# Performance work log

Measured on AMD Instinct MI355X. Metric: run time of the kernel, lower is better.

## Reference

```python
import jax, jax.numpy as jnp
import numpy as np

IN_DIM = 128
NUM_KERNELS = 512
OUT_DIM = 256
EPS_NORM = 1e-09


def setup_inputs() -> dict:
    key = jax.random.key(0)
    k1, k2, k3, k4 = jax.random.split(key, 4)
    inp = jax.random.normal(k1, (16, 512, IN_DIM), dtype=jnp.float32)
    # centers ~ U[-1, 1] as in reset(upper_bound_kernels=1.0)
    centers = jax.random.uniform(k2, (NUM_KERNELS, IN_DIM), dtype=jnp.float32, minval=-1.0, maxval=1.0)
    # log shapes ~ N(0, 0.1)
    log_shapes = 0.1 * jax.random.normal(k3, (NUM_KERNELS,), dtype=jnp.float32)
    # xavier-uniform weights, gain=1: bound = sqrt(6/(fan_in+fan_out))
    bound = float(np.sqrt(6.0 / (NUM_KERNELS + OUT_DIM)))
    weights = jax.random.uniform(k4, (OUT_DIM, NUM_KERNELS), dtype=jnp.float32, minval=-bound, maxval=bound)
    return {"input": inp, "kernels_centers": centers, "log_shapes": log_shapes, "weights": weights}


def reference(input, kernels_centers, log_shapes, weights):
    lead = input.shape[:-1]
    x = input.reshape(-1, input.shape[-1])            # (N, D)
    diff = x[:, None, :] - kernels_centers[None, :, :]  # (N, K, D)
    r = jnp.linalg.norm(diff, axis=-1)                 # (N, K)
    eps_r = jnp.exp(log_shapes)[None, :] * r           # (N, K)
    rbfs = jnp.exp(-eps_r ** 2)                        # gaussian RBF
    rbfs = rbfs / (jnp.sum(rbfs, axis=-1, keepdims=True) + EPS_NORM)
    out = rbfs @ weights.T                             # (N, OUT)
    return out.reshape(lead + (weights.shape[0],))
```

## Files before the change

### kernel.cpp

```cpp
#include <hip/hip_runtime.h>

typedef float  f32x4 __attribute__((ext_vector_type(4)));
typedef short  s16x8 __attribute__((ext_vector_type(8)));
typedef ushort u16x8 __attribute__((ext_vector_type(8)));

constexpr int D  = 128;
constexpr int K  = 512;
constexpr int O  = 256;
constexpr int NT = 256;
constexpr float NL2E = -1.44269504088896340736f;

__device__ __forceinline__ ushort f2bf(float f) {
    uint u = __builtin_bit_cast(uint, f);
    return (ushort)((u + 0x7FFFu + ((u >> 16) & 1u)) >> 16);
}
__device__ __forceinline__ float bf2f(ushort h) {
    return __builtin_bit_cast(float, ((uint)h) << 16);
}

__global__ __launch_bounds__(NT)
void rbf_prep(const float* __restrict__ x, const float* __restrict__ cen,
              const float* __restrict__ ls, const float* __restrict__ w,
              ushort* __restrict__ Xh, ushort* __restrict__ Xl,
              ushort* __restrict__ Ch, ushort* __restrict__ Cl,
              ushort* __restrict__ Wf, float* __restrict__ xs2,
              float2* __restrict__ ecs, int nxb, int ncb)
{
    __shared__ float red[4][16];
    const int b = blockIdx.x, t = threadIdx.x, lane = t & 63, wq = t >> 6;

    if (b < nxb + ncb) {
        const bool isX  = b < nxb;
        const int panel = isX ? b : (b - nxb);
        const float* src = isX ? x : cen;
        ushort* dh = isX ? Xh : Ch;
        ushort* dl = isX ? Xl : Cl;
        const int row = panel * 16 + (lane & 15);
        const int col = wq * 32 + (lane >> 4) * 8;
        const float* p = src + (size_t)row * D + col;
        float4 v0 = *(const float4*)p, v1 = *(const float4*)(p + 4);
        float f[8] = {v0.x, v0.y, v0.z, v0.w, v1.x, v1.y, v1.z, v1.w};
        u16x8 h, l;
        float s = 0.f;
#pragma unroll
        for (int j = 0; j < 8; ++j) {
            s = fmaf(f[j], f[j], s);
            ushort hb = f2bf(f[j]);
            h[j] = hb;
            l[j] = f2bf(f[j] - bf2f(hb));
        }
        const size_t c = ((size_t)panel * 4 + wq) * 64 + lane;
        *(u16x8*)&dh[c * 8] = h;
        *(u16x8*)&dl[c * 8] = l;
        s += __shfl_xor(s, 16);
        s += __shfl_xor(s, 32);
        if (lane < 16) red[wq][lane] = s;
        __syncthreads();
        if (t < 16) {
            float sum = red[0][t] + red[1][t] + red[2][t] + red[3][t];
            if (isX) {
                xs2[panel * 16 + t] = sum;
            } else {
                int k = panel * 16 + t;
                float e = __expf(2.0f * ls[k]);
                ecs[k] = make_float2(NL2E * e, NL2E * e * sum);
            }
        }
    } else {
        const int c0 = (b - nxb - ncb) * NT + t;
        const int ln = c0 & 63, ot = (c0 >> 6) & 15, ks = c0 >> 10;
        const int o  = ot * 16 + (ln & 15);
        const int kb = ks * 32 + (ln >> 4) * 8;
        const float* p = w + (size_t)o * K + kb;
        float4 v0 = *(const float4*)p, v1 = *(const float4*)(p + 4);
        u16x8 h;
        h[0] = f2bf(v0.x); h[1] = f2bf(v0.y); h[2] = f2bf(v0.z); h[3] = f2bf(v0.w);
        h[4] = f2bf(v1.x); h[5] = f2bf(v1.y); h[6] = f2bf(v1.z); h[7] = f2bf(v1.w);
        *(u16x8*)&Wf[(size_t)c0 * 8] = h;
    }
}

constexpr int PP = 40;

__global__ __launch_bounds__(512, 1)
void rbf_main2p(const ushort* __restrict__ Xh, const ushort* __restrict__ Xl,
                const ushort* __restrict__ Ch, const ushort* __restrict__ Cl,
                const ushort* __restrict__ Wf, const float* __restrict__ xs2,
                const float2* __restrict__ ecs, float* __restrict__ out, int N)
{
    __shared__ ushort PsA[8][16][PP];
    __shared__ ushort PsB[8][16][PP];
    __shared__ float  Acc[2][32][O + 4];
    __shared__ float  Ls[8][32];

    const int t = threadIdx.x, lane = t & 63, wv = t >> 6;
    const int l15 = lane & 15, l4 = lane >> 4;
    const int pan = blockIdx.x;

    s16x8 xhA[4], xlA[4], xhB[4], xlB[4];
    {
        const size_t baseA = ((size_t)(pan * 2) * 4) * 64 + lane;
        const size_t baseB = ((size_t)(pan * 2 + 1) * 4) * 64 + lane;
#pragma unroll
        for (int q = 0; q < 4; ++q) {
            xhA[q] = *(const s16x8*)&Xh[(baseA + q * 64) * 8];
            xlA[q] = *(const s16x8*)&Xl[(baseA + q * 64) * 8];
            xhB[q] = *(const s16x8*)&Xh[(baseB + q * 64) * 8];
            xlB[q] = *(const s16x8*)&Xl[(baseB + q * 64) * 8];
        }
    }
    const float xs2A = xs2[pan * 32 + l15];
    const float xs2B = xs2[pan * 32 + 16 + l15];

    f32x4 oaccA[16], oaccB[16];
#pragma unroll
    for (int i = 0; i < 16; ++i) {
        oaccA[i] = (f32x4){0.f, 0.f, 0.f, 0.f};
        oaccB[i] = (f32x4){0.f, 0.f, 0.f, 0.f};
    }
    float LpA = 0.f, LpB = 0.f;

    const int kw = wv * 64;

#pragma unroll
    for (int s = 0; s < 2; ++s) {
        const int kslab = (kw >> 5) + s;
        const ushort* wbase = &Wf[(((size_t)kslab * 16) * 64 + lane) * 8];

#pragma unroll
        for (int bt = 0; bt < 2; ++bt) {
            const size_t kt16 = (size_t)(kw >> 4) + s * 2 + bt;
            s16x8 ch[4], cl[4];
#pragma unroll
            for (int q = 0; q < 4; ++q) {
                const size_t cc = ((kt16 * 4 + q) * 64 + lane) * 8;
                ch[q] = *(const s16x8*)&Ch[cc];
                cl[q] = *(const s16x8*)&Cl[cc];
            }
            f32x4 gA = (f32x4){0.f,0.f,0.f,0.f};
            f32x4 gB = (f32x4){0.f,0.f,0.f,0.f};
#pragma unroll
            for (int q = 0; q < 4; ++q) {
                gA = __builtin_amdgcn_mfma_f32_16x16x32_bf16(ch[q], xhA[q], gA, 0, 0, 0);
                gB = __builtin_amdgcn_mfma_f32_16x16x32_bf16(ch[q], xhB[q], gB, 0, 0, 0);
            }
#pragma unroll
            for (int q = 0; q < 4; ++q) {
                gA = __builtin_amdgcn_mfma_f32_16x16x32_bf16(ch[q], xlA[q], gA, 0, 0, 0);
                gB = __builtin_amdgcn_mfma_f32_16x16x32_bf16(ch[q], xlB[q], gB, 0, 0, 0);
            }
#pragma unroll
            for (int q = 0; q < 4; ++q) {
                gA = __builtin_amdgcn_mfma_f32_16x16x32_bf16(cl[q], xhA[q], gA, 0, 0, 0);
                gB = __builtin_amdgcn_mfma_f32_16x16x32_bf16(cl[q], xhB[q], gB, 0, 0, 0);
            }

            const int kbase = kw + s * 32 + bt * 16 + l4 * 4;
            float4 e0 = *(const float4*)&ecs[kbase];
            float4 e1 = *(const float4*)&ecs[kbase + 2];
            {
                float p0 = exp2f(fmaf(e0.x, fmaf(-2.f, gA[0], xs2A), e0.y));
                float p1 = exp2f(fmaf(e0.z, fmaf(-2.f, gA[1], xs2A), e0.w));
                float p2 = exp2f(fmaf(e1.x, fmaf(-2.f, gA[2], xs2A), e1.y));
                float p3 = exp2f(fmaf(e1.z, fmaf(-2.f, gA[3], xs2A), e1.w));
                LpA += (p0 + p1) + (p2 + p3);
                uint u0 = (uint)f2bf(p0) | ((uint)f2bf(p1) << 16);
                uint u1 = (uint)f2bf(p2) | ((uint)f2bf(p3) << 16);
                *(uint2*)&PsA[wv][l15][bt * 16 + l4 * 4] = make_uint2(u0, u1);
            }
            {
                float p0 = exp2f(fmaf(e0.x, fmaf(-2.f, gB[0], xs2B), e0.y));
                float p1 = exp2f(fmaf(e0.z, fmaf(-2.f, gB[1], xs2B), e0.w));
                float p2 = exp2f(fmaf(e1.x, fmaf(-2.f, gB[2], xs2B), e1.y));
                float p3 = exp2f(fmaf(e1.z, fmaf(-2.f, gB[3], xs2B), e1.w));
                LpB += (p0 + p1) + (p2 + p3);
                uint u0 = (uint)f2bf(p0) | ((uint)f2bf(p1) << 16);
                uint u1 = (uint)f2bf(p2) | ((uint)f2bf(p3) << 16);
                *(uint2*)&PsB[wv][l15][bt * 16 + l4 * 4] = make_uint2(u0, u1);
            }
        }

        s16x8 paA = *(const s16x8*)&PsA[wv][l15][l4 * 8];
        s16x8 paB = *(const s16x8*)&PsB[wv][l15][l4 * 8];
#pragma unroll
        for (int ot = 0; ot < 16; ++ot) {
            s16x8 bfr = *(const s16x8*)&wbase[(size_t)ot * 64 * 8];
            oaccA[ot] = __builtin_amdgcn_mfma_f32_16x16x32_bf16(paA, bfr, oaccA[ot], 0, 0, 0);
            oaccB[ot] = __builtin_amdgcn_mfma_f32_16x16x32_bf16(paB, bfr, oaccB[ot], 0, 0, 0);
        }
    }

    {
        float vA = LpA, vB = LpB;
        vA += __shfl_xor(vA, 16);  vA += __shfl_xor(vA, 32);
        vB += __shfl_xor(vB, 16);  vB += __shfl_xor(vB, 32);
        if (lane < 16) {
            Ls[wv][lane]      = vA;
            Ls[wv][16 + lane] = vB;
        }
    }

    if (wv < 2) {
#pragma unroll
        for (int ot = 0; ot < 16; ++ot)
#pragma unroll
            for (int r = 0; r < 4; ++r) {
                Acc[wv][l4 * 4 + r][ot * 16 + l15]      = oaccA[ot][r];
                Acc[wv][16 + l4 * 4 + r][ot * 16 + l15] = oaccB[ot][r];
            }
    }
    __syncthreads();
    if (wv == 2 || wv == 3) {
#pragma unroll
        for (int ot = 0; ot < 16; ++ot)
#pragma unroll
            for (int r = 0; r < 4; ++r) {
                Acc[wv - 2][l4 * 4 + r][ot * 16 + l15]      += oaccA[ot][r];
                Acc[wv - 2][16 + l4 * 4 + r][ot * 16 + l15] += oaccB[ot][r];
            }
    }
    __syncthreads();
    if (wv == 4 || wv == 5) {
#pragma unroll
        for (int ot = 0; ot < 16; ++ot)
#pragma unroll
            for (int r = 0; r < 4; ++r) {
                Acc[wv - 4][l4 * 4 + r][ot * 16 + l15]      += oaccA[ot][r];
                Acc[wv - 4][16 + l4 * 4 + r][ot * 16 + l15] += oaccB[ot][r];
            }
    }
    __syncthreads();
    if (wv >= 6) {
#pragma unroll
        for (int ot = 0; ot < 16; ++ot)
#pragma unroll
            for (int r = 0; r < 4; ++r) {
                Acc[wv - 6][l4 * 4 + r][ot * 16 + l15]      += oaccA[ot][r];
                Acc[wv - 6][16 + l4 * 4 + r][ot * 16 + l15] += oaccB[ot][r];
            }
    }
    __syncthreads();

    {
        const int n  = t >> 4;
        const int c0 = (t & 15) * 16;
        float inv = 1.0f / (Ls[0][n] + Ls[1][n] + Ls[2][n] + Ls[3][n] +
                            Ls[4][n] + Ls[5][n] + Ls[6][n] + Ls[7][n] + 1e-9f);
        float* po = &out[(size_t)(pan * 32 + n) * O + c0];
#pragma unroll
        for (int j = 0; j < 4; ++j) {
            float4 a = *(const float4*)&Acc[0][n][c0 + j * 4];
            float4 b = *(const float4*)&Acc[1][n][c0 + j * 4];
            float4 o;
            o.x = (a.x + b.x) * inv;
            o.y = (a.y + b.y) * inv;
            o.z = (a.z + b.z) * inv;
            o.w = (a.w + b.w) * inv;
            *(float4*)(po + j * 4) = o;
        }
    }
}

__global__ __launch_bounds__(NT, 2)
void rbf_fb(const float* __restrict__ x, const float* __restrict__ cen,
            const float* __restrict__ ls, const float* __restrict__ w,
            float* __restrict__ out)
{
    __shared__ ushort Ps2[2][4][16][PP];
    __shared__ float  Acc2[2][16][O + 4];
    __shared__ float  Ls2[4][16];
    const int t = threadIdx.x, lane = t & 63, wv = t >> 6;
    const int l15 = lane & 15, l4 = lane >> 4;
    const int nb = blockIdx.x * 16;

    s16x8 xh[4], xl[4];
    float sx = 0.f;
    {
        const float* xr = x + (size_t)(nb + l15) * D;
#pragma unroll
        for (int q = 0; q < 4; ++q) {
            float4 v0 = *(const float4*)(xr + q * 32 + l4 * 8);
            float4 v1 = *(const float4*)(xr + q * 32 + l4 * 8 + 4);
            float f[8] = {v0.x, v0.y, v0.z, v0.w, v1.x, v1.y, v1.z, v1.w};
            s16x8 hh, lo;
#pragma unroll
            for (int j = 0; j < 8; ++j) {
                sx = fmaf(f[j], f[j], sx);
                ushort hb = f2bf(f[j]);
                hh[j] = (short)hb; lo[j] = (short)f2bf(f[j] - bf2f(hb));
            }
            xh[q] = hh; xl[q] = lo;
        }
    }
    sx += __shfl_xor(sx, 16); sx += __shfl_xor(sx, 32);
    float xs2v[4];
#pragma unroll
    for (int r = 0; r < 4; ++r) xs2v[r] = __shfl(sx, l4 * 4 + r);

    f32x4 oacc[16];
#pragma unroll
    for (int ot = 0; ot < 16; ++ot) oacc[ot] = (f32x4){0.f,0.f,0.f,0.f};
    float Lp[4] = {0.f,0.f,0.f,0.f};
    const int kq = wv * (K / 4);

#pragma unroll
    for (int s = 0; s < 4; ++s) {
        const int k0 = kq + s * 32;
#pragma unroll
        for (int bt = 0; bt < 2; ++bt) {
            const int kk = k0 + bt * 16 + l15;
            const float* cr = cen + (size_t)kk * D;
            s16x8 ch[4], cl[4];
            float sc = 0.f;
#pragma unroll
            for (int q = 0; q < 4; ++q) {
                float4 v0 = *(const float4*)(cr + q * 32 + l4 * 8);
                float4 v1 = *(const float4*)(cr + q * 32 + l4 * 8 + 4);
                float f[8] = {v0.x, v0.y, v0.z, v0.w, v1.x, v1.y, v1.z, v1.w};
                s16x8 hh, lo;
#pragma unroll
                for (int j = 0; j < 8; ++j) {
                    sc = fmaf(f[j], f[j], sc);
                    ushort hb = f2bf(f[j]);
                    hh[j] = (short)hb; lo[j] = (short)f2bf(f[j] - bf2f(hb));
                }
                ch[q] = hh; cl[q] = lo;
            }
            sc += __shfl_xor(sc, 16); sc += __shfl_xor(sc, 32);
            float es_ = __expf(2.0f * ls[kk]);
            f32x4 ghh={0,0,0,0}, ghl={0,0,0,0}, glh={0,0,0,0};
#pragma unroll
            for (int q = 0; q < 4; ++q) {
                ghh = __builtin_amdgcn_mfma_f32_16x16x32_bf16(xh[q], ch[q], ghh, 0,0,0);
                ghl = __builtin_amdgcn_mfma_f32_16x16x32_bf16(xh[q], cl[q], ghl, 0,0,0);
                glh = __builtin_amdgcn_mfma_f32_16x16x32_bf16(xl[q], ch[q], glh, 0,0,0);
            }
            f32x4 gg = ghh + ghl + glh;
#pragma unroll
            for (int r = 0; r < 4; ++r) {
                float r2 = xs2v[r] + sc - 2.0f * gg[r];
                float ph = __expf(-es_ * r2);
                Lp[r] += ph;
                Ps2[s & 1][wv][l4 * 4 + r][bt * 16 + l15] = f2bf(ph);
            }
        }
        s16x8 pa = *(const s16x8*)&Ps2[s & 1][wv][l15][l4 * 8];
#pragma unroll
        for (int ot = 0; ot < 16; ++ot) {
            const float* wr = w + (size_t)(ot * 16 + l15) * K + k0;
            float4 v0 = *(const float4*)(wr + l4 * 8);
            float4 v1 = *(const float4*)(wr + l4 * 8 + 4);
            s16x8 bb;
            bb[0]=(short)f2bf(v0.x); bb[1]=(short)f2bf(v0.y); bb[2]=(short)f2bf(v0.z); bb[3]=(short)f2bf(v0.w);
            bb[4]=(short)f2bf(v1.x); bb[5]=(short)f2bf(v1.y); bb[6]=(short)f2bf(v1.z); bb[7]=(short)f2bf(v1.w);
            oacc[ot] = __builtin_amdgcn_mfma_f32_16x16x32_bf16(pa, bb, oacc[ot], 0,0,0);
        }
    }
#pragma unroll
    for (int r = 0; r < 4; ++r) {
        float v = Lp[r];
        v += __shfl_xor(v, 1); v += __shfl_xor(v, 2);
        v += __shfl_xor(v, 4); v += __shfl_xor(v, 8);
        if (l15 == 0) Ls2[wv][l4 * 4 + r] = v;
    }
    if (wv < 2) {
#pragma unroll
        for (int ot = 0; ot < 16; ++ot)
#pragma unroll
            for (int r = 0; r < 4; ++r)
                Acc2[wv][l4 * 4 + r][ot * 16 + l15] = oacc[ot][r];
    }
    __syncthreads();
    if (wv >= 2) {
#pragma unroll
        for (int ot = 0; ot < 16; ++ot)
#pragma unroll
            for (int r = 0; r < 4; ++r)
                Acc2[wv - 2][l4 * 4 + r][ot * 16 + l15] += oacc[ot][r];
    }
    __syncthreads();
#pragma unroll
    for (int rr = 0; rr < 4; ++rr) {
        const int n = wv * 4 + rr;
        float inv = 1.0f / (Ls2[0][n] + Ls2[1][n] + Ls2[2][n] + Ls2[3][n] + 1e-9f);
        float4 a0 = *(const float4*)&Acc2[0][n][lane * 4];
        float4 a1 = *(const float4*)&Acc2[1][n][lane * 4];
        float4 o4;
        o4.x = (a0.x + a1.x) * inv; o4.y = (a0.y + a1.y) * inv;
        o4.z = (a0.z + a1.z) * inv; o4.w = (a0.w + a1.w) * inv;
        *(float4*)&out[(size_t)(nb + n) * O + lane * 4] = o4;
    }
}

extern "C" void kernel_launch(void* const* d_in, const int* in_sizes, int n_in,
                              void* d_out, int out_size, void* d_ws, size_t ws_size,
                              hipStream_t stream) {
    const float* x   = (const float*)d_in[0];
    const float* cen = (const float*)d_in[1];
    const float* ls  = (const float*)d_in[2];
    const float* w   = (const float*)d_in[3];
    float* out = (float*)d_out;
    const int N = in_sizes[0] / D;

    size_t oXh = 0;
    size_t oXl = oXh + (size_t)N * D * 2;
    size_t oCh = oXl + (size_t)N * D * 2;
    size_t oCl = oCh + (size_t)K * D * 2;
    size_t oWf = oCl + (size_t)K * D * 2;
    size_t oxs = oWf + (size_t)O * K * 2;
    size_t oec = oxs + (size_t)N * 4;
    size_t need = oec + (size_t)K * 8;

    if (ws_size < need || (N % 32) != 0) {
        dim3 grid(N / 16), block(NT);
        hipLaunchKernelGGL(rbf_fb, grid, block, 0, stream, x, cen, ls, w, out);
        return;
    }

    char* ws = (char*)d_ws;
    ushort* Xh = (ushort*)(ws + oXh);
    ushort* Xl = (ushort*)(ws + oXl);
    ushort* Ch = (ushort*)(ws + oCh);
    ushort* Cl = (ushort*)(ws + oCl);
    ushort* Wf = (ushort*)(ws + oWf);
    float*  xs2 = (float*)(ws + oxs);
    float2* ecs = (float2*)(ws + oec);

    const int nxb = N / 16;
    const int ncb = K / 16;
    const int nwb = (O * K / 8) / NT;
    dim3 pgrid(nxb + ncb + nwb), pblock(NT);
    hipLaunchKernelGGL(rbf_prep, pgrid, pblock, 0, stream,
                       x, cen, ls, w, Xh, Xl, Ch, Cl, Wf, xs2, ecs, nxb, ncb);

    dim3 grid(N / 32), block(512);
    hipLaunchKernelGGL(rbf_main2p, grid, block, 0, stream,
                       Xh, Xl, Ch, Cl, Wf, xs2, ecs, out, N);
}
```

Measured before the change: 27.76 us.

## Fuse prep and main kernels into one cooperative kernel with grid sync

Merges the preprocessing kernel (bf16 hi/lo splitting of inputs and centers, squared norms, weight conversion) and the main RBF/GEMM kernel into a single cooperative launch separated by a grid-wide barrier. This removes one kernel launch and the gap between the two kernels. The cooperative path is hardcoded to N=8192 (256 blocks, 608 prep jobs), and falls back to the two-kernel path if the cooperative launch fails. It depends on all 256 blocks of 512 threads being co-resident, and the grid sync adds its own cost.

```diff
diff --git a/kernel.cpp b/kernel.cpp
--- a/kernel.cpp
+++ b/kernel.cpp
@@ -1,4 +1,7 @@
 #include <hip/hip_runtime.h>
+#include <hip/hip_cooperative_groups.h>
+
+namespace cg = cooperative_groups;
 
 typedef float  f32x4 __attribute__((ext_vector_type(4)));
 typedef short  s16x8 __attribute__((ext_vector_type(8)));
@@ -16,6 +19,250 @@
 }
 __device__ __forceinline__ float bf2f(ushort h) {
     return __builtin_bit_cast(float, ((uint)h) << 16);
+}
+
+constexpr int PP = 40;
+
+__global__ __launch_bounds__(512, 1)
+void rbf_coop(const float* __restrict__ x, const float* __restrict__ cen,
+              const float* __restrict__ ls, const float* __restrict__ w,
+              ushort* __restrict__ Xh, ushort* __restrict__ Xl,
+              ushort* __restrict__ Ch, ushort* __restrict__ Cl,
+              ushort* __restrict__ Wf, float* __restrict__ xs2,
+              float2* __restrict__ ecs, float* __restrict__ out, int N)
+{
+    __shared__ ushort PsA[8][16][PP];
+    __shared__ ushort PsB[8][16][PP];
+    __shared__ float  Acc[2][32][O + 4];
+    __shared__ float  Ls[8][32];
+
+    const int tt = threadIdx.x;
+
+    {
+        const int hb   = blockIdx.x * 2 + (tt >> 8);
+        const int tloc = tt & 255;
+        const int wj = (tloc >> 6);
+        const int lj = tloc & 63;
+        const int rr = lj >> 4;
+        const int cb = lj & 15;
+        for (int job = hb; job < 608; job += 512) {
+            if (job < 544) {
+                const bool isX = job < 512;
+                const int panel = isX ? job : job - 512;
+                const float* src = isX ? x : cen;
+                ushort* dh = isX ? Xh : Ch;
+                ushort* dl = isX ? Xl : Cl;
+                const int row = panel * 16 + wj * 4 + rr;
+                const float* p = src + (size_t)row * D + cb * 8;
+                float4 v0 = *(const float4*)p, v1 = *(const float4*)(p + 4);
+                float f[8] = {v0.x, v0.y, v0.z, v0.w, v1.x, v1.y, v1.z, v1.w};
+                u16x8 h, l;
+                float s = 0.f;
+#pragma unroll
+                for (int j = 0; j < 8; ++j) {
+                    s = fmaf(f[j], f[j], s);
+                    ushort hb2 = f2bf(f[j]);
+                    h[j] = hb2;
+                    l[j] = f2bf(f[j] - bf2f(hb2));
+                }
+                const int q  = cb >> 2;
+                const int lp = (wj * 4 + rr) + (cb & 3) * 16;
+                const size_t c = ((size_t)panel * 4 + q) * 64 + lp;
+                *(u16x8*)&dh[c * 8] = h;
+                *(u16x8*)&dl[c * 8] = l;
+                s += __shfl_xor(s, 1); s += __shfl_xor(s, 2);
+                s += __shfl_xor(s, 4); s += __shfl_xor(s, 8);
+                if (cb == 0) {
+                    if (isX) {
+                        xs2[row] = s;
+                    } else {
+                        float e = __expf(2.0f * ls[row]);
+                        ecs[row] = make_float2(NL2E * e, NL2E * e * s);
+                    }
+                }
+            } else {
+                const int c0 = (job - 544) * 256 + tloc;
+                const int ln = c0 & 63, ot = (c0 >> 6) & 15, ks = c0 >> 10;
+                const int o  = ot * 16 + (ln & 15);
+                const int kb = ks * 32 + (ln >> 4) * 8;
+                const float* p = w + (size_t)o * K + kb;
+                float4 v0 = *(const float4*)p, v1 = *(const float4*)(p + 4);
+                u16x8 h;
+                h[0] = f2bf(v0.x); h[1] = f2bf(v0.y); h[2] = f2bf(v0.z); h[3] = f2bf(v0.w);
+                h[4] = f2bf(v1.x); h[5] = f2bf(v1.y); h[6] = f2bf(v1.z); h[7] = f2bf(v1.w);
+                *(u16x8*)&Wf[(size_t)c0 * 8] = h;
+            }
+        }
+    }
+
+    cg::this_grid().sync();
+
+    const int lane = tt & 63, wv = tt >> 6;
+    const int l15 = lane & 15, l4 = lane >> 4;
+    const int pan = blockIdx.x;
+
+    s16x8 xhA[4], xlA[4], xhB[4], xlB[4];
+    {
+        const size_t baseA = ((size_t)(pan * 2) * 4) * 64 + lane;
+        const size_t baseB = ((size_t)(pan * 2 + 1) * 4) * 64 + lane;
+#pragma unroll
+        for (int q = 0; q < 4; ++q) {
+            xhA[q] = *(const s16x8*)&Xh[(baseA + q * 64) * 8];
+            xlA[q] = *(const s16x8*)&Xl[(baseA + q * 64) * 8];
+            xhB[q] = *(const s16x8*)&Xh[(baseB + q * 64) * 8];
+            xlB[q] = *(const s16x8*)&Xl[(baseB + q * 64) * 8];
+        }
+    }
+    const float xs2A = xs2[pan * 32 + l15];
+    const float xs2B = xs2[pan * 32 + 16 + l15];
+
+    f32x4 oaccA[16], oaccB[16];
+#pragma unroll
+    for (int i = 0; i < 16; ++i) {
+        oaccA[i] = (f32x4){0.f, 0.f, 0.f, 0.f};
+        oaccB[i] = (f32x4){0.f, 0.f, 0.f, 0.f};
+    }
+    float LpA = 0.f, LpB = 0.f;
+
+    const int kw = wv * 64;
+
+#pragma unroll
+    for (int s = 0; s < 2; ++s) {
+        const int kslab = (kw >> 5) + s;
+        const ushort* wbase = &Wf[(((size_t)kslab * 16) * 64 + lane) * 8];
+
+#pragma unroll
+        for (int bt = 0; bt < 2; ++bt) {
+            const size_t kt16 = (size_t)(kw >> 4) + s * 2 + bt;
+            s16x8 ch[4], cl[4];
+#pragma unroll
+            for (int q = 0; q < 4; ++q) {
+                const size_t cc = ((kt16 * 4 + q) * 64 + lane) * 8;
+                ch[q] = *(const s16x8*)&Ch[cc];
+                cl[q] = *(const s16x8*)&Cl[cc];
+            }
+            f32x4 gA = (f32x4){0.f,0.f,0.f,0.f};
+            f32x4 gB = (f32x4){0.f,0.f,0.f,0.f};
+#pragma unroll
+            for (int q = 0; q < 4; ++q) {
+                gA = __builtin_amdgcn_mfma_f32_16x16x32_bf16(ch[q], xhA[q], gA, 0, 0, 0);
+                gB = __builtin_amdgcn_mfma_f32_16x16x32_bf16(ch[q], xhB[q], gB, 0, 0, 0);
+            }
+#pragma unroll
+            for (int q = 0; q < 4; ++q) {
+                gA = __builtin_amdgcn_mfma_f32_16x16x32_bf16(ch[q], xlA[q], gA, 0, 0, 0);
+                gB = __builtin_amdgcn_mfma_f32_16x16x32_bf16(ch[q], xlB[q], gB, 0, 0, 0);
+            }
+#pragma unroll
+            for (int q = 0; q < 4; ++q) {
+                gA = __builtin_amdgcn_mfma_f32_16x16x32_bf16(cl[q], xhA[q], gA, 0, 0, 0);
+                gB = __builtin_amdgcn_mfma_f32_16x16x32_bf16(cl[q], xhB[q], gB, 0, 0, 0);
+            }
+
+            const int kbase = kw + s * 32 + bt * 16 + l4 * 4;
+            float4 e0 = *(const float4*)&ecs[kbase];
+            float4 e1 = *(const float4*)&ecs[kbase + 2];
+            {
+                float p0 = exp2f(fmaf(e0.x, fmaf(-2.f, gA[0], xs2A), e0.y));
+                float p1 = exp2f(fmaf(e0.z, fmaf(-2.f, gA[1], xs2A), e0.w));
+                float p2 = exp2f(fmaf(e1.x, fmaf(-2.f, gA[2], xs2A), e1.y));
+                float p3 = exp2f(fmaf(e1.z, fmaf(-2.f, gA[3], xs2A), e1.w));
+                LpA += (p0 + p1) + (p2 + p3);
+                uint u0 = (uint)f2bf(p0) | ((uint)f2bf(p1) << 16);
+                uint u1 = (uint)f2bf(p2) | ((uint)f2bf(p3) << 16);
+                *(uint2*)&PsA[wv][l15][bt * 16 + l4 * 4] = make_uint2(u0, u1);
+            }
+            {
+                float p0 = exp2f(fmaf(e0.x, fmaf(-2.f, gB[0], xs2B), e0.y));
+                float p1 = exp2f(fmaf(e0.z, fmaf(-2.f, gB[1], xs2B), e0.w));
+                float p2 = exp2f(fmaf(e1.x, fmaf(-2.f, gB[2], xs2B), e1.y));
+                float p3 = exp2f(fmaf(e1.z, fmaf(-2.f, gB[3], xs2B), e1.w));
+                LpB += (p0 + p1) + (p2 + p3);
+                uint u0 = (uint)f2bf(p0) | ((uint)f2bf(p1) << 16);
+                uint u1 = (uint)f2bf(p2) | ((uint)f2bf(p3) << 16);
+                *(uint2*)&PsB[wv][l15][bt * 16 + l4 * 4] = make_uint2(u0, u1);
+            }
+        }
+
+        s16x8 paA = *(const s16x8*)&PsA[wv][l15][l4 * 8];
+        s16x8 paB = *(const s16x8*)&PsB[wv][l15][l4 * 8];
+#pragma unroll
+        for (int ot = 0; ot < 16; ++ot) {
+            s16x8 bfr = *(const s16x8*)&wbase[(size_t)ot * 64 * 8];
+            oaccA[ot] = __builtin_amdgcn_mfma_f32_16x16x32_bf16(paA, bfr, oaccA[ot], 0, 0, 0);
+            oaccB[ot] = __builtin_amdgcn_mfma_f32_16x16x32_bf16(paB, bfr, oaccB[ot], 0, 0, 0);
+        }
+    }
+
+    {
+        float vA = LpA, vB = LpB;
+        vA += __shfl_xor(vA, 16);  vA += __shfl_xor(vA, 32);
+        vB += __shfl_xor(vB, 16);  vB += __shfl_xor(vB, 32);
+        if (lane < 16) {
+            Ls[wv][lane]      = vA;
+            Ls[wv][16 + lane] = vB;
+        }
+    }
+
+    if (wv < 2) {
+#pragma unroll
+        for (int ot = 0; ot < 16; ++ot)
+#pragma unroll
+            for (int r = 0; r < 4; ++r) {
+                Acc[wv][l4 * 4 + r][ot * 16 + l15]      = oaccA[ot][r];
+                Acc[wv][16 + l4 * 4 + r][ot * 16 + l15] = oaccB[ot][r];
+            }
+    }
+    __syncthreads();
+    if (wv == 2 || wv == 3) {
+#pragma unroll
+        for (int ot = 0; ot < 16; ++ot)
+#pragma unroll
+            for (int r = 0; r < 4; ++r) {
+                Acc[wv - 2][l4 * 4 + r][ot * 16 + l15]      += oaccA[ot][r];
+                Acc[wv - 2][16 + l4 * 4 + r][ot * 16 + l15] += oaccB[ot][r];
+            }
+    }
+    __syncthreads();
+    if (wv == 4 || wv == 5) {
+#pragma unroll
+        for (int ot = 0; ot < 16; ++ot)
+#pragma unroll
+            for (int r = 0; r < 4; ++r) {
+                Acc[wv - 4][l4 * 4 + r][ot * 16 + l15]      += oaccA[ot][r];
+                Acc[wv - 4][16 + l4 * 4 + r][ot * 16 + l15] += oaccB[ot][r];
+            }
+    }
+    __syncthreads();
+    if (wv >= 6) {
+#pragma unroll
+        for (int ot = 0; ot < 16; ++ot)
+#pragma unroll
+            for (int r = 0; r < 4; ++r) {
+                Acc[wv - 6][l4 * 4 + r][ot * 16 + l15]      += oaccA[ot][r];
+                Acc[wv - 6][16 + l4 * 4 + r][ot * 16 + l15] += oaccB[ot][r];
+            }
+    }
+    __syncthreads();
+
+    {
+        const int n  = tt >> 4;
+        const int c0 = (tt & 15) * 16;
+        float inv = 1.0f / (Ls[0][n] + Ls[1][n] + Ls[2][n] + Ls[3][n] +
+                            Ls[4][n] + Ls[5][n] + Ls[6][n] + Ls[7][n] + 1e-9f);
+        float* po = &out[(size_t)(pan * 32 + n) * O + c0];
+#pragma unroll
+        for (int j = 0; j < 4; ++j) {
+            float4 a = *(const float4*)&Acc[0][n][c0 + j * 4];
+            float4 b = *(const float4*)&Acc[1][n][c0 + j * 4];
+            float4 o;
+            o.x = (a.x + b.x) * inv;
+            o.y = (a.y + b.y) * inv;
+            o.z = (a.z + b.z) * inv;
+            o.w = (a.w + b.w) * inv;
+            *(float4*)(po + j * 4) = o;
+        }
+    }
 }
 
 __global__ __launch_bounds__(NT)
@@ -80,8 +327,6 @@
     }
 }
 
-constexpr int PP = 40;
-
 __global__ __launch_bounds__(512, 1)
 void rbf_main2p(const ushort* __restrict__ Xh, const ushort* __restrict__ Xl,
                 const ushort* __restrict__ Ch, const ushort* __restrict__ Cl,
@@ -411,7 +656,7 @@
     size_t oec = oxs + (size_t)N * 4;
     size_t need = oec + (size_t)K * 8;
 
-    if (ws_size < need || (N % 32) != 0) {
+    if (ws_size < need || N != 8192) {
         dim3 grid(N / 16), block(NT);
         hipLaunchKernelGGL(rbf_fb, grid, block, 0, stream, x, cen, ls, w, out);
         return;
@@ -426,6 +671,19 @@
     float*  xs2 = (float*)(ws + oxs);
     float2* ecs = (float2*)(ws + oec);
 
+    {
+        int Nv = N;
+        void* params[] = { (void*)&x, (void*)&cen, (void*)&ls, (void*)&w,
+                           (void*)&Xh, (void*)&Xl, (void*)&Ch, (void*)&Cl,
+                           (void*)&Wf, (void*)&xs2, (void*)&ecs,
+                           (void*)&out, (void*)&Nv };
+        hipError_t err = hipLaunchCooperativeKernel(
+            reinterpret_cast<void*>(&rbf_coop), dim3(N / 32), dim3(512),
+            params, 0, stream);
+        if (err == hipSuccess) return;
+        (void)hipGetLastError();
+    }
+
     const int nxb = N / 16;
     const int ncb = K / 16;
     const int nwb = (O * K / 8) / NT;
```

Result: slower. 66.26 us (+138.7%).

## Fuse bf16 prep into main kernel, converting inputs on the fly

Applied to the files above, without the earlier changes.

Drops the separate prep kernel and its workspace buffers. The main kernel now reads fp32 x, centers and weights directly and splits them into bf16 hi/lo in registers. The x low part is shared through LDS, and norms and shape factors are computed in place and passed around with lane shuffles. This removes one launch and a global round trip, but every block now redoes the center and weight conversion and reads fp32 data, twice the bytes of bf16.

```diff
diff --git a/kernel.cpp b/kernel.cpp
--- a/kernel.cpp
+++ b/kernel.cpp
@@ -9,6 +9,7 @@
 constexpr int O  = 256;
 constexpr int NT = 256;
 constexpr float NL2E = -1.44269504088896340736f;
+constexpr int PP = 40;
 
 __device__ __forceinline__ ushort f2bf(float f) {
     uint u = __builtin_bit_cast(uint, f);
@@ -18,76 +19,12 @@
     return __builtin_bit_cast(float, ((uint)h) << 16);
 }
 
-__global__ __launch_bounds__(NT)
-void rbf_prep(const float* __restrict__ x, const float* __restrict__ cen,
-              const float* __restrict__ ls, const float* __restrict__ w,
-              ushort* __restrict__ Xh, ushort* __restrict__ Xl,
-              ushort* __restrict__ Ch, ushort* __restrict__ Cl,
-              ushort* __restrict__ Wf, float* __restrict__ xs2,
-              float2* __restrict__ ecs, int nxb, int ncb)
+__global__ __launch_bounds__(512, 1)
+void rbf_fused1(const float* __restrict__ x, const float* __restrict__ cen,
+                const float* __restrict__ ls, const float* __restrict__ w,
+                float* __restrict__ out)
 {
-    __shared__ float red[4][16];
-    const int b = blockIdx.x, t = threadIdx.x, lane = t & 63, wq = t >> 6;
-
-    if (b < nxb + ncb) {
-        const bool isX  = b < nxb;
-        const int panel = isX ? b : (b - nxb);
-        const float* src = isX ? x : cen;
-        ushort* dh = isX ? Xh : Ch;
-        ushort* dl = isX ? Xl : Cl;
-        const int row = panel * 16 + (lane & 15);
-        const int col = wq * 32 + (lane >> 4) * 8;
-        const float* p = src + (size_t)row * D + col;
-        float4 v0 = *(const float4*)p, v1 = *(const float4*)(p + 4);
-        float f[8] = {v0.x, v0.y, v0.z, v0.w, v1.x, v1.y, v1.z, v1.w};
-        u16x8 h, l;
-        float s = 0.f;
-#pragma unroll
-        for (int j = 0; j < 8; ++j) {
-            s = fmaf(f[j], f[j], s);
-            ushort hb = f2bf(f[j]);
-            h[j] = hb;
-            l[j] = f2bf(f[j] - bf2f(hb));
-        }
-        const size_t c = ((size_t)panel * 4 + wq) * 64 + lane;
-        *(u16x8*)&dh[c * 8] = h;
-        *(u16x8*)&dl[c * 8] = l;
-        s += __shfl_xor(s, 16);
-        s += __shfl_xor(s, 32);
-        if (lane < 16) red[wq][lane] = s;
-        __syncthreads();
-        if (t < 16) {
-            float sum = red[0][t] + red[1][t] + red[2][t] + red[3][t];
-            if (isX) {
-                xs2[panel * 16 + t] = sum;
-            } else {
-                int k = panel * 16 + t;
-                float e = __expf(2.0f * ls[k]);
-                ecs[k] = make_float2(NL2E * e, NL2E * e * sum);
-            }
-        }
-    } else {
-        const int c0 = (b - nxb - ncb) * NT + t;
-        const int ln = c0 & 63, ot = (c0 >> 6) & 15, ks = c0 >> 10;
-        const int o  = ot * 16 + (ln & 15);
-        const int kb = ks * 32 + (ln >> 4) * 8;
-        const float* p = w + (size_t)o * K + kb;
-        float4 v0 = *(const float4*)p, v1 = *(const float4*)(p + 4);
-        u16x8 h;
-        h[0] = f2bf(v0.x); h[1] = f2bf(v0.y); h[2] = f2bf(v0.z); h[3] = f2bf(v0.w);
-        h[4] = f2bf(v1.x); h[5] = f2bf(v1.y); h[6] = f2bf(v1.z); h[7] = f2bf(v1.w);
-        *(u16x8*)&Wf[(size_t)c0 * 8] = h;
-    }
-}
-
-constexpr int PP = 40;
-
-__global__ __launch_bounds__(512, 1)
-void rbf_main2p(const ushort* __restrict__ Xh, const ushort* __restrict__ Xl,
-                const ushort* __restrict__ Ch, const ushort* __restrict__ Cl,
-                const ushort* __restrict__ Wf, const float* __restrict__ xs2,
-                const float2* __restrict__ ecs, float* __restrict__ out, int N)
-{
+    __shared__ ushort XloL[2][4][64][8];
     __shared__ ushort PsA[8][16][PP];
     __shared__ ushort PsB[8][16][PP];
     __shared__ float  Acc[2][32][O + 4];
@@ -96,21 +33,49 @@
     const int t = threadIdx.x, lane = t & 63, wv = t >> 6;
     const int l15 = lane & 15, l4 = lane >> 4;
     const int pan = blockIdx.x;
-
-    s16x8 xhA[4], xlA[4], xhB[4], xlB[4];
+    const int nb  = pan * 32;
+
+    s16x8 xhA[4], xhB[4];
+    float sxA = 0.f, sxB = 0.f;
     {
-        const size_t baseA = ((size_t)(pan * 2) * 4) * 64 + lane;
-        const size_t baseB = ((size_t)(pan * 2 + 1) * 4) * 64 + lane;
+        const float* xrA = x + (size_t)(nb + l15) * D + l4 * 8;
+        const float* xrB = x + (size_t)(nb + 16 + l15) * D + l4 * 8;
 #pragma unroll
         for (int q = 0; q < 4; ++q) {
-            xhA[q] = *(const s16x8*)&Xh[(baseA + q * 64) * 8];
-            xlA[q] = *(const s16x8*)&Xl[(baseA + q * 64) * 8];
-            xhB[q] = *(const s16x8*)&Xh[(baseB + q * 64) * 8];
-            xlB[q] = *(const s16x8*)&Xl[(baseB + q * 64) * 8];
-        }
-    }
-    const float xs2A = xs2[pan * 32 + l15];
-    const float xs2B = xs2[pan * 32 + 16 + l15];
+            float4 a0 = *(const float4*)(xrA + q * 32);
+            float4 a1 = *(const float4*)(xrA + q * 32 + 4);
+            float4 b0 = *(const float4*)(xrB + q * 32);
+            float4 b1 = *(const float4*)(xrB + q * 32 + 4);
+            float fa[8] = {a0.x,a0.y,a0.z,a0.w,a1.x,a1.y,a1.z,a1.w};
+            float fb[8] = {b0.x,b0.y,b0.z,b0.w,b1.x,b1.y,b1.z,b1.w};
+            s16x8 ha, hb;
+#pragma unroll
+            for (int j = 0; j < 8; ++j) {
+                sxA = fmaf(fa[j], fa[j], sxA);
+                sxB = fmaf(fb[j], fb[j], sxB);
+                ha[j] = (short)f2bf(fa[j]);
+                hb[j] = (short)f2bf(fb[j]);
+            }
+            xhA[q] = ha; xhB[q] = hb;
+            if (wv == 0) {
+                u16x8 la, lb;
+#pragma unroll
+                for (int j = 0; j < 8; ++j) {
+                    la[j] = f2bf(fa[j] - bf2f((ushort)ha[j]));
+                    lb[j] = f2bf(fb[j] - bf2f((ushort)hb[j]));
+                }
+                *(u16x8*)&XloL[0][q][lane][0] = la;
+                *(u16x8*)&XloL[1][q][lane][0] = lb;
+            }
+        }
+    }
+    sxA += __shfl_xor(sxA, 16);  sxA += __shfl_xor(sxA, 32);
+    sxB += __shfl_xor(sxB, 16);  sxB += __shfl_xor(sxB, 32);
+
+    const int kw = wv * 64;
+    const float nev = NL2E * __expf(2.0f * ls[kw + lane]);
+
+    __syncthreads();
 
     f32x4 oaccA[16], oaccB[16];
 #pragma unroll
@@ -120,23 +85,36 @@
     }
     float LpA = 0.f, LpB = 0.f;
 
-    const int kw = wv * 64;
-
-#pragma unroll
-    for (int s = 0; s < 2; ++s) {
-        const int kslab = (kw >> 5) + s;
-        const ushort* wbase = &Wf[(((size_t)kslab * 16) * 64 + lane) * 8];
+#pragma unroll
+    for (int s2 = 0; s2 < 2; ++s2) {
+        const int kslab = (kw >> 5) + s2;
 
 #pragma unroll
         for (int bt = 0; bt < 2; ++bt) {
-            const size_t kt16 = (size_t)(kw >> 4) + s * 2 + bt;
+            const int tloc = s2 * 2 + bt;
+            const int krow = kw + tloc * 16 + l15;
+            const float* cr = cen + (size_t)krow * D + l4 * 8;
+
             s16x8 ch[4], cl[4];
-#pragma unroll
-            for (int q = 0; q < 4; ++q) {
-                const size_t cc = ((kt16 * 4 + q) * 64 + lane) * 8;
-                ch[q] = *(const s16x8*)&Ch[cc];
-                cl[q] = *(const s16x8*)&Cl[cc];
-            }
+            float sc = 0.f;
+#pragma unroll
+            for (int q = 0; q < 4; ++q) {
+                float4 v0 = *(const float4*)(cr + q * 32);
+                float4 v1 = *(const float4*)(cr + q * 32 + 4);
+                float f[8] = {v0.x,v0.y,v0.z,v0.w,v1.x,v1.y,v1.z,v1.w};
+                s16x8 hh, lo;
+#pragma unroll
+                for (int j = 0; j < 8; ++j) {
+                    sc = fmaf(f[j], f[j], sc);
+                    ushort hb = f2bf(f[j]);
+                    hh[j] = (short)hb;
+                    lo[j] = (short)f2bf(f[j] - bf2f(hb));
+                }
+                ch[q] = hh; cl[q] = lo;
+            }
+            sc += __shfl_xor(sc, 16);
+            sc += __shfl_xor(sc, 32);
+
             f32x4 gA = (f32x4){0.f,0.f,0.f,0.f};
             f32x4 gB = (f32x4){0.f,0.f,0.f,0.f};
 #pragma unroll
@@ -146,8 +124,10 @@
             }
 #pragma unroll
             for (int q = 0; q < 4; ++q) {
-                gA = __builtin_amdgcn_mfma_f32_16x16x32_bf16(ch[q], xlA[q], gA, 0, 0, 0);
-                gB = __builtin_amdgcn_mfma_f32_16x16x32_bf16(ch[q], xlB[q], gB, 0, 0, 0);
+                s16x8 xa = *(const s16x8*)&XloL[0][q][lane][0];
+                s16x8 xb = *(const s16x8*)&XloL[1][q][lane][0];
+                gA = __builtin_amdgcn_mfma_f32_16x16x32_bf16(ch[q], xa, gA, 0, 0, 0);
+                gB = __builtin_amdgcn_mfma_f32_16x16x32_bf16(ch[q], xb, gB, 0, 0, 0);
             }
 #pragma unroll
             for (int q = 0; q < 4; ++q) {
@@ -155,24 +135,30 @@
                 gB = __builtin_amdgcn_mfma_f32_16x16x32_bf16(cl[q], xhB[q], gB, 0, 0, 0);
             }
 
-            const int kbase = kw + s * 32 + bt * 16 + l4 * 4;
-            float4 e0 = *(const float4*)&ecs[kbase];
-            float4 e1 = *(const float4*)&ecs[kbase + 2];
+            const int li0 = tloc * 16 + l4 * 4;
+            float ne0 = __shfl(nev, li0 + 0);
+            float ne1 = __shfl(nev, li0 + 1);
+            float ne2 = __shfl(nev, li0 + 2);
+            float ne3 = __shfl(nev, li0 + 3);
+            float c20 = __shfl(sc, l4 * 4 + 0);
+            float c21 = __shfl(sc, l4 * 4 + 1);
+            float c22 = __shfl(sc, l4 * 4 + 2);
+            float c23 = __shfl(sc, l4 * 4 + 3);
             {
-                float p0 = exp2f(fmaf(e0.x, fmaf(-2.f, gA[0], xs2A), e0.y));
-                float p1 = exp2f(fmaf(e0.z, fmaf(-2.f, gA[1], xs2A), e0.w));
-                float p2 = exp2f(fmaf(e1.x, fmaf(-2.f, gA[2], xs2A), e1.y));
-                float p3 = exp2f(fmaf(e1.z, fmaf(-2.f, gA[3], xs2A), e1.w));
+                float p0 = exp2f(ne0 * fmaf(-2.f, gA[0], sxA + c20));
+                float p1 = exp2f(ne1 * fmaf(-2.f, gA[1], sxA + c21));
+                float p2 = exp2f(ne2 * fmaf(-2.f, gA[2], sxA + c22));
+                float p3 = exp2f(ne3 * fmaf(-2.f, gA[3], sxA + c23));
                 LpA += (p0 + p1) + (p2 + p3);
                 uint u0 = (uint)f2bf(p0) | ((uint)f2bf(p1) << 16);
                 uint u1 = (uint)f2bf(p2) | ((uint)f2bf(p3) << 16);
                 *(uint2*)&PsA[wv][l15][bt * 16 + l4 * 4] = make_uint2(u0, u1);
             }
             {
-                float p0 = exp2f(fmaf(e0.x, fmaf(-2.f, gB[0], xs2B), e0.y));
-                float p1 = exp2f(fmaf(e0.z, fmaf(-2.f, gB[1], xs2B), e0.w));
-                float p2 = exp2f(fmaf(e1.x, fmaf(-2.f, gB[2], xs2B), e1.y));
-                float p3 = exp2f(fmaf(e1.z, fmaf(-2.f, gB[3], xs2B), e1.w));
+                float p0 = exp2f(ne0 * fmaf(-2.f, gB[0], sxB + c20));
+                float p1 = exp2f(ne1 * fmaf(-2.f, gB[1], sxB + c21));
+                float p2 = exp2f(ne2 * fmaf(-2.f, gB[2], sxB + c22));
+                float p3 = exp2f(ne3 * fmaf(-2.f, gB[3], sxB + c23));
                 LpB += (p0 + p1) + (p2 + p3);
                 uint u0 = (uint)f2bf(p0) | ((uint)f2bf(p1) << 16);
                 uint u1 = (uint)f2bf(p2) | ((uint)f2bf(p3) << 16);
@@ -184,9 +170,16 @@
         s16x8 paB = *(const s16x8*)&PsB[wv][l15][l4 * 8];
 #pragma unroll
         for (int ot = 0; ot < 16; ++ot) {
-            s16x8 bfr = *(const s16x8*)&wbase[(size_t)ot * 64 * 8];
-            oaccA[ot] = __builtin_amdgcn_mfma_f32_16x16x32_bf16(paA, bfr, oaccA[ot], 0, 0, 0);
-            oaccB[ot] = __builtin_amdgcn_mfma_f32_16x16x32_bf16(paB, bfr, oaccB[ot], 0, 0, 0);
+            const float* wr = w + (size_t)(ot * 16 + l15) * K + kslab * 32 + l4 * 8;
+            float4 v0 = *(const float4*)wr;
+            float4 v1 = *(const float4*)(wr + 4);
+            s16x8 bb;
+            bb[0]=(short)f2bf(v0.x); bb[1]=(short)f2bf(v0.y);
+            bb[2]=(short)f2bf(v0.z); bb[3]=(short)f2bf(v0.w);
+            bb[4]=(short)f2bf(v1.x); bb[5]=(short)f2bf(v1.y);
+            bb[6]=(short)f2bf(v1.z); bb[7]=(short)f2bf(v1.w);
+            oaccA[ot] = __builtin_amdgcn_mfma_f32_16x16x32_bf16(paA, bb, oaccA[ot], 0, 0, 0);
+            oaccB[ot] = __builtin_amdgcn_mfma_f32_16x16x32_bf16(paB, bb, oaccB[ot], 0, 0, 0);
         }
     }
 
@@ -246,7 +239,7 @@
         const int c0 = (t & 15) * 16;
         float inv = 1.0f / (Ls[0][n] + Ls[1][n] + Ls[2][n] + Ls[3][n] +
                             Ls[4][n] + Ls[5][n] + Ls[6][n] + Ls[7][n] + 1e-9f);
-        float* po = &out[(size_t)(pan * 32 + n) * O + c0];
+        float* po = &out[(size_t)(nb + n) * O + c0];
 #pragma unroll
         for (int j = 0; j < 4; ++j) {
             float4 a = *(const float4*)&Acc[0][n][c0 + j * 4];
@@ -402,38 +395,12 @@
     float* out = (float*)d_out;
     const int N = in_sizes[0] / D;
 
-    size_t oXh = 0;
-    size_t oXl = oXh + (size_t)N * D * 2;
-    size_t oCh = oXl + (size_t)N * D * 2;
-    size_t oCl = oCh + (size_t)K * D * 2;
-    size_t oWf = oCl + (size_t)K * D * 2;
-    size_t oxs = oWf + (size_t)O * K * 2;
-    size_t oec = oxs + (size_t)N * 4;
-    size_t need = oec + (size_t)K * 8;
-
-    if (ws_size < need || (N % 32) != 0) {
+    if ((N % 32) != 0) {
         dim3 grid(N / 16), block(NT);
         hipLaunchKernelGGL(rbf_fb, grid, block, 0, stream, x, cen, ls, w, out);
         return;
     }
 
-    char* ws = (char*)d_ws;
-    ushort* Xh = (ushort*)(ws + oXh);
-    ushort* Xl = (ushort*)(ws + oXl);
-    ushort* Ch = (ushort*)(ws + oCh);
-    ushort* Cl = (ushort*)(ws + oCl);
-    ushort* Wf = (ushort*)(ws + oWf);
-    float*  xs2 = (float*)(ws + oxs);
-    float2* ecs = (float2*)(ws + oec);
-
-    const int nxb = N / 16;
-    const int ncb = K / 16;
-    const int nwb = (O * K / 8) / NT;
-    dim3 pgrid(nxb + ncb + nwb), pblock(NT);
-    hipLaunchKernelGGL(rbf_prep, pgrid, pblock, 0, stream,
-                       x, cen, ls, w, Xh, Xl, Ch, Cl, Wf, xs2, ecs, nxb, ncb);
-
     dim3 grid(N / 32), block(512);
-    hipLaunchKernelGGL(rbf_main2p, grid, block, 0, stream,
-                       Xh, Xl, Ch, Cl, Wf, xs2, ecs, out, N);
+    hipLaunchKernelGGL(rbf_fused1, grid, block, 0, stream, x, cen, ls, w, out);
 }
```

Measured after the change: 45.12 us. +62.5%, slower.
